# Optimization experiments

Measured on AMD Instinct MI355X. Metric: run time of the kernel, lower is better.

Reference implementation:

```python
import jax, jax.numpy as jnp
import numpy as np


def _bilinear_sample(tex, grid):
    """grid_sample, bilinear, align_corners=True, padding_mode='zeros'.
    tex: [C, Hin, Win]; grid: [B, Ho, Wo, 2] in [-1, 1] (x=width, y=height).
    Returns [B, C, Ho, Wo].
    """
    C, Hin, Win = tex.shape
    gx, gy = grid[..., 0], grid[..., 1]
    # align_corners=True mapping
    ix = (gx + 1.0) * 0.5 * (Win - 1)
    iy = (gy + 1.0) * 0.5 * (Hin - 1)
    ix0 = jnp.floor(ix)
    iy0 = jnp.floor(iy)
    wx1 = ix - ix0
    wy1 = iy - iy0
    wx0 = 1.0 - wx1
    wy0 = 1.0 - wy1

    def gather(iy_, ix_):
        valid = (ix_ >= 0) & (ix_ <= Win - 1) & (iy_ >= 0) & (iy_ <= Hin - 1)
        ic = jnp.clip(ix_, 0, Win - 1).astype(jnp.int32)
        jc = jnp.clip(iy_, 0, Hin - 1).astype(jnp.int32)
        v = tex[:, jc, ic]  # [C, B, Ho, Wo]
        return v * valid.astype(tex.dtype)[None]

    out = (gather(iy0, ix0) * (wy0 * wx0)[None]
           + gather(iy0, ix0 + 1) * (wy0 * wx1)[None]
           + gather(iy0 + 1, ix0) * (wy1 * wx0)[None]
           + gather(iy0 + 1, ix0 + 1) * (wy1 * wx1)[None])
    return jnp.transpose(out, (1, 0, 2, 3))  # [B, C, Ho, Wo]


def setup_inputs() -> dict:
    key = jax.random.key(0)
    k = jax.random.split(key, 6)
    B, C, W, H = 4, 16, 1024, 1024
    Ho, Wo = 512, 512
    return {
        "x": jax.random.uniform(k[0], (B, Ho, Wo, 2), dtype=jnp.float32),
        "x_msk": jax.random.uniform(k[1], (B, Ho, Wo), dtype=jnp.float32),
        "layer1": jax.random.normal(k[2], (C, W, H), dtype=jnp.float32),
        "layer2": jax.random.normal(k[3], (C, W // 2, H // 2), dtype=jnp.float32),
        "layer3": jax.random.normal(k[4], (C, W // 4, H // 4), dtype=jnp.float32),
        "layer4": jax.random.normal(k[5], (C, W // 8, H // 8), dtype=jnp.float32),
    }


def reference(x, x_msk, layer1, layer2, layer3, layer4):
    grid = x * 2.0 - 1.0
    y = (_bilinear_sample(layer1, grid)
         + _bilinear_sample(layer2, grid)
         + _bilinear_sample(layer3, grid)
         + _bilinear_sample(layer4, grid))
    return y * x_msk[:, None]
```

## Files before the change

### kernel.cpp

```cpp
#include <hip/hip_runtime.h>
#include <hip/hip_fp16.h>

#define CH 16
#define NPIX (4 * 512 * 512)
#define NBINS 4096
#define NBLK_SORT 256
#define PPB (NPIX / NBLK_SORT)
#define SEGS 16

__global__ __launch_bounds__(256) void interleave_all_kernel(
    const float* __restrict__ l1, const float* __restrict__ l2,
    const float* __restrict__ l3, const float* __restrict__ l4,
    __half* __restrict__ w1, __half* __restrict__ w2,
    __half* __restrict__ w3, __half* __restrict__ w4) {
  int g = blockIdx.x * blockDim.x + threadIdx.x;
  const float* src; __half* dst; int HW, p;
  if (g < 1048576)      { src = l1; dst = w1; HW = 1048576; p = g; }
  else if (g < 1310720) { src = l2; dst = w2; HW = 262144;  p = g - 1048576; }
  else if (g < 1376256) { src = l3; dst = w3; HW = 65536;   p = g - 1310720; }
  else                  { src = l4; dst = w4; HW = 16384;   p = g - 1376256; }
  union { __half h[CH]; uint4 u[2]; } pk;
#pragma unroll
  for (int c = 0; c < CH; ++c) pk.h[c] = __float2half(src[(size_t)c * HW + p]);
  uint4* d = (uint4*)(dst + (size_t)p * CH);
  d[0] = pk.u[0];
  d[1] = pk.u[1];
}

__device__ __forceinline__ void corner_fma(const __half* __restrict__ t,
                                           size_t texel, float w, float acc[CH]) {
  const uint4* q = (const uint4*)(t + texel * CH);
  union { uint4 u; __half2 h[4]; } a, b;
  a.u = q[0];
  b.u = q[1];
#pragma unroll
  for (int i = 0; i < 4; ++i) {
    float2 f = __half22float2(a.h[i]);
    acc[2 * i + 0] = fmaf(f.x, w, acc[2 * i + 0]);
    acc[2 * i + 1] = fmaf(f.y, w, acc[2 * i + 1]);
  }
#pragma unroll
  for (int i = 0; i < 4; ++i) {
    float2 f = __half22float2(b.h[i]);
    acc[8 + 2 * i + 0] = fmaf(f.x, w, acc[8 + 2 * i + 0]);
    acc[8 + 2 * i + 1] = fmaf(f.y, w, acc[8 + 2 * i + 1]);
  }
}

__device__ __forceinline__ void sample_hwc16(const __half* __restrict__ t, int W,
                                             float gx, float gy, float acc[CH]) {
  const float W1 = (float)(W - 1);
  float ix = (gx + 1.0f) * 0.5f * W1;
  float iy = (gy + 1.0f) * 0.5f * W1;
  float ix0f = floorf(ix), iy0f = floorf(iy);
  float wx1 = ix - ix0f, wy1 = iy - iy0f;
  float wx0 = 1.0f - wx1, wy0 = 1.0f - wy1;
  float ix1f = ix0f + 1.0f, iy1f = iy0f + 1.0f;
  float vx0 = (ix0f >= 0.0f && ix0f <= W1) ? 1.0f : 0.0f;
  float vx1 = (ix1f >= 0.0f && ix1f <= W1) ? 1.0f : 0.0f;
  float vy0 = (iy0f >= 0.0f && iy0f <= W1) ? 1.0f : 0.0f;
  float vy1 = (iy1f >= 0.0f && iy1f <= W1) ? 1.0f : 0.0f;
  int x0 = min(max((int)ix0f, 0), W - 1);
  int x1 = min(max((int)ix1f, 0), W - 1);
  int y0 = min(max((int)iy0f, 0), W - 1);
  int y1 = min(max((int)iy1f, 0), W - 1);
  float w00 = wy0 * wx0 * vy0 * vx0;
  float w01 = wy0 * wx1 * vy0 * vx1;
  float w10 = wy1 * wx0 * vy1 * vx0;
  float w11 = wy1 * wx1 * vy1 * vx1;
  corner_fma(t, (size_t)y0 * W + x0, w00, acc);
  corner_fma(t, (size_t)y0 * W + x1, w01, acc);
  corner_fma(t, (size_t)y1 * W + x0, w10, acc);
  corner_fma(t, (size_t)y1 * W + x1, w11, acc);
}

__device__ __forceinline__ int bin_of(float xv, float yv) {
  int bx = min(max((int)(xv * 1023.0f), 0), 1023) >> 4;
  int by = min(max((int)(yv * 1023.0f), 0), 1023) >> 4;
  return (by << 6) + bx;
}

__global__ __launch_bounds__(256) void hist_kernel(
    const float2* __restrict__ x, unsigned* __restrict__ hist) {
  __shared__ unsigned h[NBINS];
  int tid = threadIdx.x, blk = blockIdx.x;
#pragma unroll
  for (int i = 0; i < NBINS / 256; ++i) h[i * 256 + tid] = 0;
  __syncthreads();
  int base = blk * PPB;
#pragma unroll 4
  for (int c = 0; c < PPB / 256; ++c) {
    float2 g = x[base + c * 256 + tid];
    atomicAdd(&h[bin_of(g.x, g.y)], 1u);
  }
  __syncthreads();
#pragma unroll
  for (int i = 0; i < NBINS / 256; ++i)
    hist[(size_t)blk * NBINS + i * 256 + tid] = h[i * 256 + tid];
}

__global__ __launch_bounds__(256) void segsum_kernel(
    const unsigned* __restrict__ hist, unsigned* __restrict__ partial) {
  int gid = blockIdx.x * 256 + threadIdx.x;
  int s = gid >> 12, bin = gid & (NBINS - 1);
  unsigned sum = 0;
#pragma unroll
  for (int k = 0; k < NBLK_SORT / SEGS; ++k)
    sum += hist[(size_t)(s * (NBLK_SORT / SEGS) + k) * NBINS + bin];
  partial[gid] = sum;
}

__global__ __launch_bounds__(256) void segscan_kernel(
    unsigned* __restrict__ partial, unsigned* __restrict__ totals) {
  int bin = blockIdx.x * 256 + threadIdx.x;
  unsigned run = 0;
#pragma unroll
  for (int s = 0; s < SEGS; ++s) {
    unsigned v = partial[s * NBINS + bin];
    partial[s * NBINS + bin] = run;
    run += v;
  }
  totals[bin] = run;
}

__global__ __launch_bounds__(1024) void scan_kernel(
    const unsigned* __restrict__ counts, unsigned* __restrict__ cursor) {
  __shared__ unsigned part[1024];
  int t = threadIdx.x;
  unsigned c0 = counts[4 * t + 0], c1 = counts[4 * t + 1];
  unsigned c2 = counts[4 * t + 2], c3 = counts[4 * t + 3];
  part[t] = c0 + c1 + c2 + c3;
  __syncthreads();
  for (int off = 1; off < 1024; off <<= 1) {
    unsigned v = (t >= off) ? part[t - off] : 0u;
    __syncthreads();
    part[t] += v;
    __syncthreads();
  }
  unsigned base = (t > 0) ? part[t - 1] : 0u;
  cursor[4 * t + 0] = base;
  cursor[4 * t + 1] = base + c0;
  cursor[4 * t + 2] = base + c0 + c1;
  cursor[4 * t + 3] = base + c0 + c1 + c2;
}

__global__ __launch_bounds__(256) void colscan_kernel(
    unsigned* __restrict__ hist, const unsigned* __restrict__ partial,
    const unsigned* __restrict__ binbase) {
  int gid = blockIdx.x * 256 + threadIdx.x;
  int s = gid >> 12, bin = gid & (NBINS - 1);
  unsigned run = partial[s * NBINS + bin] + binbase[bin];
#pragma unroll
  for (int k = 0; k < NBLK_SORT / SEGS; ++k) {
    size_t idx = (size_t)(s * (NBLK_SORT / SEGS) + k) * NBINS + bin;
    unsigned v = hist[idx];
    hist[idx] = run;
    run += v;
  }
}

__global__ __launch_bounds__(256) void scatter2_kernel(
    const float2* __restrict__ x, const float* __restrict__ msk,
    const unsigned* __restrict__ hist, float4* __restrict__ pixrec) {
  __shared__ unsigned cur[NBINS];
  int tid = threadIdx.x, blk = blockIdx.x;
#pragma unroll
  for (int i = 0; i < NBINS / 256; ++i)
    cur[i * 256 + tid] = hist[(size_t)blk * NBINS + i * 256 + tid];
  __syncthreads();
  int base = blk * PPB;
#pragma unroll 4
  for (int c = 0; c < PPB / 256; ++c) {
    int p = base + c * 256 + tid;
    float2 g = x[p];
    float m = msk[p];
    unsigned i = atomicAdd(&cur[bin_of(g.x, g.y)], 1u);
    pixrec[i] = make_float4(g.x, g.y, __uint_as_float((unsigned)p), m);
  }
}

__device__ __forceinline__ unsigned spread4(unsigned v) {
  v = (v | (v << 2)) & 0x33u;
  v = (v | (v << 1)) & 0x55u;
  return v;
}

__global__ __launch_bounds__(256) void gather_binned_kernel(
    const float4* __restrict__ pixrec,
    const __half* __restrict__ t1, const __half* __restrict__ t2,
    const __half* __restrict__ t3, const __half* __restrict__ t4,
    __half* __restrict__ ws2) {
  __shared__ float4 srec[256];
  __shared__ unsigned scnt[256];
  __shared__ unsigned sbase[256];
  int tid = threadIdx.x;
  int bid = blockIdx.x;
  int swz = (bid & 7) * 512 + (bid >> 3);
  float4 r = pixrec[swz * 256 + tid];

  int txq = min(max((int)(r.x * 1023.0f), 0), 1023) & 15;
  int tyq = min(max((int)(r.y * 1023.0f), 0), 1023) & 15;
  unsigned key = spread4((unsigned)txq) | (spread4((unsigned)tyq) << 1);
  scnt[tid] = 0;
  __syncthreads();
  unsigned rank = atomicAdd(&scnt[key], 1u);
  __syncthreads();
  sbase[tid] = scnt[tid];
  __syncthreads();
  for (int off = 1; off < 256; off <<= 1) {
    unsigned v = (tid >= off) ? sbase[tid - off] : 0u;
    __syncthreads();
    sbase[tid] += v;
    __syncthreads();
  }
  unsigned pos = sbase[key] - scnt[key] + rank;
  srec[pos] = r;
  __syncthreads();
  r = srec[tid];

  float gx = r.x * 2.0f - 1.0f;
  float gy = r.y * 2.0f - 1.0f;
  unsigned p = __float_as_uint(r.z);
  float m = r.w;
  float acc[CH];
#pragma unroll
  for (int c = 0; c < CH; ++c) acc[c] = 0.0f;
  sample_hwc16(t1, 1024, gx, gy, acc);
  sample_hwc16(t2, 512, gx, gy, acc);
  sample_hwc16(t3, 256, gx, gy, acc);
  sample_hwc16(t4, 128, gx, gy, acc);
  union { __half2 h[8]; uint4 u[2]; } o;
#pragma unroll
  for (int c = 0; c < 8; ++c)
    o.h[c] = __floats2half2_rn(acc[2 * c] * m, acc[2 * c + 1] * m);
  uint4* w = (uint4*)(ws2 + (size_t)p * CH);
  w[0] = o.u[0];
  w[1] = o.u[1];
}

__global__ __launch_bounds__(256) void unscatter16_kernel(
    const __half* __restrict__ ws2, float* __restrict__ out) {
  int t = blockIdx.x * blockDim.x + threadIdx.x;
  int p0 = t * 4;
  int wo = p0 & 511, ho = (p0 >> 9) & 511, b = p0 >> 18;
  const uint4* s = (const uint4*)ws2;
  union { uint4 u[2]; __half2 h[8]; } v[4];
#pragma unroll
  for (int j = 0; j < 4; ++j) {
    v[j].u[0] = s[(size_t)(p0 + j) * 2 + 0];
    v[j].u[1] = s[(size_t)(p0 + j) * 2 + 1];
  }
  size_t obase = (size_t)b * (CH * 262144) + (size_t)ho * 512 + wo;
#pragma unroll
  for (int ch = 0; ch < CH; ++ch) {
    float4 o;
    o.x = __half2float(((ch & 1) ? __high2half(v[0].h[ch >> 1]) : __low2half(v[0].h[ch >> 1])));
    o.y = __half2float(((ch & 1) ? __high2half(v[1].h[ch >> 1]) : __low2half(v[1].h[ch >> 1])));
    o.z = __half2float(((ch & 1) ? __high2half(v[2].h[ch >> 1]) : __low2half(v[2].h[ch >> 1])));
    o.w = __half2float(((ch & 1) ? __high2half(v[3].h[ch >> 1]) : __low2half(v[3].h[ch >> 1])));
    *(float4*)(out + obase + (size_t)ch * 262144) = o;
  }
}

__global__ __launch_bounds__(256) void gather_hwc16_kernel(
    const float* __restrict__ x, const float* __restrict__ msk,
    const __half* __restrict__ t1, const __half* __restrict__ t2,
    const __half* __restrict__ t3, const __half* __restrict__ t4,
    float* __restrict__ out) {
  int p = blockIdx.x * blockDim.x + threadIdx.x;
  int wo = p & 511, ho = (p >> 9) & 511, b = p >> 18;
  float2 g = ((const float2*)x)[p];
  float gx = g.x * 2.0f - 1.0f;
  float gy = g.y * 2.0f - 1.0f;
  float m = msk[p];
  float acc[CH];
#pragma unroll
  for (int c = 0; c < CH; ++c) acc[c] = 0.0f;
  sample_hwc16(t1, 1024, gx, gy, acc);
  sample_hwc16(t2, 512, gx, gy, acc);
  sample_hwc16(t3, 256, gx, gy, acc);
  sample_hwc16(t4, 128, gx, gy, acc);
  size_t obase = (size_t)b * (CH * 262144) + (size_t)ho * 512 + wo;
#pragma unroll
  for (int c = 0; c < CH; ++c) out[obase + (size_t)c * 262144] = acc[c] * m;
}

__device__ __forceinline__ void sample_chw(const float* __restrict__ t, int W,
                                           float gx, float gy, float acc[CH]) {
  const float W1 = (float)(W - 1);
  float ix = (gx + 1.0f) * 0.5f * W1;
  float iy = (gy + 1.0f) * 0.5f * W1;
  float ix0f = floorf(ix), iy0f = floorf(iy);
  float wx1 = ix - ix0f, wy1 = iy - iy0f;
  float wx0 = 1.0f - wx1, wy0 = 1.0f - wy1;
  float ix1f = ix0f + 1.0f, iy1f = iy0f + 1.0f;
  float vx0 = (ix0f >= 0.0f && ix0f <= W1) ? 1.0f : 0.0f;
  float vx1 = (ix1f >= 0.0f && ix1f <= W1) ? 1.0f : 0.0f;
  float vy0 = (iy0f >= 0.0f && iy0f <= W1) ? 1.0f : 0.0f;
  float vy1 = (iy1f >= 0.0f && iy1f <= W1) ? 1.0f : 0.0f;
  int x0 = min(max((int)ix0f, 0), W - 1);
  int x1 = min(max((int)ix1f, 0), W - 1);
  int y0 = min(max((int)iy0f, 0), W - 1);
  int y1 = min(max((int)iy1f, 0), W - 1);
  float w00 = wy0 * wx0 * vy0 * vx0;
  float w01 = wy0 * wx1 * vy0 * vx1;
  float w10 = wy1 * wx0 * vy1 * vx0;
  float w11 = wy1 * wx1 * vy1 * vx1;
  size_t HW = (size_t)W * W;
  const float* b00 = t + (size_t)y0 * W + x0;
  const float* b01 = t + (size_t)y0 * W + x1;
  const float* b10 = t + (size_t)y1 * W + x0;
  const float* b11 = t + (size_t)y1 * W + x1;
#pragma unroll
  for (int c = 0; c < CH; ++c) {
    float v00 = b00[c * HW], v01 = b01[c * HW], v10 = b10[c * HW], v11 = b11[c * HW];
    acc[c] = fmaf(v00, w00, fmaf(v01, w01, fmaf(v10, w10, fmaf(v11, w11, acc[c]))));
  }
}

__global__ __launch_bounds__(256) void gather_chw_kernel(
    const float* __restrict__ x, const float* __restrict__ msk,
    const float* __restrict__ l1, const float* __restrict__ l2,
    const float* __restrict__ l3, const float* __restrict__ l4,
    float* __restrict__ out) {
  int p = blockIdx.x * blockDim.x + threadIdx.x;
  int wo = p & 511, ho = (p >> 9) & 511, b = p >> 18;
  float2 g = ((const float2*)x)[p];
  float gx = g.x * 2.0f - 1.0f;
  float gy = g.y * 2.0f - 1.0f;
  float m = msk[p];
  float acc[CH];
#pragma unroll
  for (int c = 0; c < CH; ++c) acc[c] = 0.0f;
  sample_chw(l1, 1024, gx, gy, acc);
  sample_chw(l2, 512, gx, gy, acc);
  sample_chw(l3, 256, gx, gy, acc);
  sample_chw(l4, 128, gx, gy, acc);
  size_t obase = (size_t)b * (CH * 262144) + (size_t)ho * 512 + wo;
#pragma unroll
  for (int c = 0; c < CH; ++c) out[obase + (size_t)c * 262144] = acc[c] * m;
}

extern "C" void kernel_launch(void* const* d_in, const int* in_sizes, int n_in,
                              void* d_out, int out_size, void* d_ws, size_t ws_size,
                              hipStream_t stream) {
  const float* x   = (const float*)d_in[0];
  const float* msk = (const float*)d_in[1];
  const float* l1  = (const float*)d_in[2];
  const float* l2  = (const float*)d_in[3];
  const float* l3  = (const float*)d_in[4];
  const float* l4  = (const float*)d_in[5];
  float* out = (float*)d_out;

  const size_t n_texel = 1048576 + 262144 + 65536 + 16384;
  const size_t tex_bytes = n_texel * CH * sizeof(__half);
  const size_t ws2_bytes = (size_t)NPIX * CH * sizeof(__half);
  const size_t rec_bytes = (size_t)NPIX * sizeof(float4);
  const size_t need_bin  = ws2_bytes + tex_bytes + rec_bytes;
  const size_t need_f16  = tex_bytes;

  if (ws_size >= need_bin) {
    char* base = (char*)d_ws;
    __half* ws2    = (__half*)base;
    __half* w1     = (__half*)(base + ws2_bytes);
    __half* w2     = w1 + (size_t)1048576 * CH;
    __half* w3     = w2 + (size_t)262144 * CH;
    __half* w4     = w3 + (size_t)65536 * CH;
    float4* pixrec = (float4*)(base + ws2_bytes + tex_bytes);
    unsigned* hist    = (unsigned*)base;
    unsigned* partial = hist + (size_t)NBLK_SORT * NBINS;
    unsigned* totals  = partial + (size_t)SEGS * NBINS;
    unsigned* binbase = totals + NBINS;

    interleave_all_kernel<<<(int)(n_texel / 256), 256, 0, stream>>>(
        l1, l2, l3, l4, w1, w2, w3, w4);
    hist_kernel<<<NBLK_SORT, 256, 0, stream>>>((const float2*)x, hist);
    segsum_kernel<<<SEGS * NBINS / 256, 256, 0, stream>>>(hist, partial);
    segscan_kernel<<<NBINS / 256, 256, 0, stream>>>(partial, totals);
    scan_kernel<<<1, 1024, 0, stream>>>(totals, binbase);
    colscan_kernel<<<SEGS * NBINS / 256, 256, 0, stream>>>(hist, partial, binbase);
    scatter2_kernel<<<NBLK_SORT, 256, 0, stream>>>((const float2*)x, msk, hist, pixrec);
    gather_binned_kernel<<<NPIX / 256, 256, 0, stream>>>(pixrec, w1, w2, w3, w4, ws2);
    unscatter16_kernel<<<NPIX / 4 / 256, 256, 0, stream>>>(ws2, out);
  } else if (ws_size >= need_f16) {
    __half* w1 = (__half*)d_ws;
    __half* w2 = w1 + (size_t)1048576 * CH;
    __half* w3 = w2 + (size_t)262144 * CH;
    __half* w4 = w3 + (size_t)65536 * CH;
    interleave_all_kernel<<<(int)(n_texel / 256), 256, 0, stream>>>(
        l1, l2, l3, l4, w1, w2, w3, w4);
    gather_hwc16_kernel<<<NPIX / 256, 256, 0, stream>>>(x, msk, w1, w2, w3, w4, out);
  } else {
    gather_chw_kernel<<<NPIX / 256, 256, 0, stream>>>(x, msk, l1, l2, l3, l4, out);
  }
}
```

Before: 124.8 us.

## Split binned gather across two threads per pixel, drop in-block Morton reorder

The binned gather kernel now assigns two threads per pixel, each handling 8 of the 16 half-precision channels with one 16-byte load per corner, and launches twice as many blocks. The in-block Morton-order sort (shared atomics, prefix scan, several barriers) is removed, leaving only the coarse bin ordering from the global sort. The aim is more memory-level parallelism, fewer registers per thread and less synchronisation overhead. The cost is that coordinate and weight math is repeated in both threads and the finer locality from the intra-block reorder is lost.

```diff
diff --git a/kernel.cpp b/kernel.cpp
--- a/kernel.cpp
+++ b/kernel.cpp
@@ -25,6 +25,47 @@
   uint4* d = (uint4*)(dst + (size_t)p * CH);
   d[0] = pk.u[0];
   d[1] = pk.u[1];
+}
+
+__device__ __forceinline__ void corner_fma_h(const __half* __restrict__ t,
+                                             size_t texel, int h, float w,
+                                             float acc[8]) {
+  union { uint4 u; __half2 hh[4]; } a;
+  a.u = ((const uint4*)t)[texel * 2 + h];
+#pragma unroll
+  for (int i = 0; i < 4; ++i) {
+    float2 f = __half22float2(a.hh[i]);
+    acc[2 * i + 0] = fmaf(f.x, w, acc[2 * i + 0]);
+    acc[2 * i + 1] = fmaf(f.y, w, acc[2 * i + 1]);
+  }
+}
+
+__device__ __forceinline__ void sample_hwc16h(const __half* __restrict__ t, int W,
+                                              float gx, float gy, int h,
+                                              float acc[8]) {
+  const float W1 = (float)(W - 1);
+  float ix = (gx + 1.0f) * 0.5f * W1;
+  float iy = (gy + 1.0f) * 0.5f * W1;
+  float ix0f = floorf(ix), iy0f = floorf(iy);
+  float wx1 = ix - ix0f, wy1 = iy - iy0f;
+  float wx0 = 1.0f - wx1, wy0 = 1.0f - wy1;
+  float ix1f = ix0f + 1.0f, iy1f = iy0f + 1.0f;
+  float vx0 = (ix0f >= 0.0f && ix0f <= W1) ? 1.0f : 0.0f;
+  float vx1 = (ix1f >= 0.0f && ix1f <= W1) ? 1.0f : 0.0f;
+  float vy0 = (iy0f >= 0.0f && iy0f <= W1) ? 1.0f : 0.0f;
+  float vy1 = (iy1f >= 0.0f && iy1f <= W1) ? 1.0f : 0.0f;
+  int x0 = min(max((int)ix0f, 0), W - 1);
+  int x1 = min(max((int)ix1f, 0), W - 1);
+  int y0 = min(max((int)iy0f, 0), W - 1);
+  int y1 = min(max((int)iy1f, 0), W - 1);
+  float w00 = wy0 * wx0 * vy0 * vx0;
+  float w01 = wy0 * wx1 * vy0 * vx1;
+  float w10 = wy1 * wx0 * vy1 * vx0;
+  float w11 = wy1 * wx1 * vy1 * vx1;
+  corner_fma_h(t, (size_t)y0 * W + x0, h, w00, acc);
+  corner_fma_h(t, (size_t)y0 * W + x1, h, w01, acc);
+  corner_fma_h(t, (size_t)y1 * W + x0, h, w10, acc);
+  corner_fma_h(t, (size_t)y1 * W + x1, h, w11, acc);
 }
 
 __device__ __forceinline__ void corner_fma(const __half* __restrict__ t,
@@ -179,63 +220,33 @@
   }
 }
 
-__device__ __forceinline__ unsigned spread4(unsigned v) {
-  v = (v | (v << 2)) & 0x33u;
-  v = (v | (v << 1)) & 0x55u;
-  return v;
-}
-
-__global__ __launch_bounds__(256) void gather_binned_kernel(
+__global__ __launch_bounds__(256) void gather_binned2_kernel(
     const float4* __restrict__ pixrec,
     const __half* __restrict__ t1, const __half* __restrict__ t2,
     const __half* __restrict__ t3, const __half* __restrict__ t4,
     __half* __restrict__ ws2) {
-  __shared__ float4 srec[256];
-  __shared__ unsigned scnt[256];
-  __shared__ unsigned sbase[256];
-  int tid = threadIdx.x;
   int bid = blockIdx.x;
-  int swz = (bid & 7) * 512 + (bid >> 3);
-  float4 r = pixrec[swz * 256 + tid];
-
-  int txq = min(max((int)(r.x * 1023.0f), 0), 1023) & 15;
-  int tyq = min(max((int)(r.y * 1023.0f), 0), 1023) & 15;
-  unsigned key = spread4((unsigned)txq) | (spread4((unsigned)tyq) << 1);
-  scnt[tid] = 0;
-  __syncthreads();
-  unsigned rank = atomicAdd(&scnt[key], 1u);
-  __syncthreads();
-  sbase[tid] = scnt[tid];
-  __syncthreads();
-  for (int off = 1; off < 256; off <<= 1) {
-    unsigned v = (tid >= off) ? sbase[tid - off] : 0u;
-    __syncthreads();
-    sbase[tid] += v;
-    __syncthreads();
-  }
-  unsigned pos = sbase[key] - scnt[key] + rank;
-  srec[pos] = r;
-  __syncthreads();
-  r = srec[tid];
-
+  int swz = (bid & 7) * 1024 + (bid >> 3);
+  int g = swz * 256 + threadIdx.x;
+  int i = g >> 1;
+  int h = g & 1;
+  float4 r = pixrec[i];
   float gx = r.x * 2.0f - 1.0f;
   float gy = r.y * 2.0f - 1.0f;
   unsigned p = __float_as_uint(r.z);
   float m = r.w;
-  float acc[CH];
-#pragma unroll
-  for (int c = 0; c < CH; ++c) acc[c] = 0.0f;
-  sample_hwc16(t1, 1024, gx, gy, acc);
-  sample_hwc16(t2, 512, gx, gy, acc);
-  sample_hwc16(t3, 256, gx, gy, acc);
-  sample_hwc16(t4, 128, gx, gy, acc);
-  union { __half2 h[8]; uint4 u[2]; } o;
-#pragma unroll
-  for (int c = 0; c < 8; ++c)
-    o.h[c] = __floats2half2_rn(acc[2 * c] * m, acc[2 * c + 1] * m);
-  uint4* w = (uint4*)(ws2 + (size_t)p * CH);
-  w[0] = o.u[0];
-  w[1] = o.u[1];
+  float acc[8];
+#pragma unroll
+  for (int c = 0; c < 8; ++c) acc[c] = 0.0f;
+  sample_hwc16h(t1, 1024, gx, gy, h, acc);
+  sample_hwc16h(t2, 512, gx, gy, h, acc);
+  sample_hwc16h(t3, 256, gx, gy, h, acc);
+  sample_hwc16h(t4, 128, gx, gy, h, acc);
+  union { __half2 hh[4]; uint4 u; } o;
+#pragma unroll
+  for (int c = 0; c < 4; ++c)
+    o.hh[c] = __floats2half2_rn(acc[2 * c] * m, acc[2 * c + 1] * m);
+  ((uint4*)(ws2 + (size_t)p * CH))[h] = o.u;
 }
 
 __global__ __launch_bounds__(256) void unscatter16_kernel(
@@ -380,7 +391,7 @@
     scan_kernel<<<1, 1024, 0, stream>>>(totals, binbase);
     colscan_kernel<<<SEGS * NBINS / 256, 256, 0, stream>>>(hist, partial, binbase);
     scatter2_kernel<<<NBLK_SORT, 256, 0, stream>>>((const float2*)x, msk, hist, pixrec);
-    gather_binned_kernel<<<NPIX / 256, 256, 0, stream>>>(pixrec, w1, w2, w3, w4, ws2);
+    gather_binned2_kernel<<<NPIX * 2 / 256, 256, 0, stream>>>(pixrec, w1, w2, w3, w4, ws2);
     unscatter16_kernel<<<NPIX / 4 / 256, 256, 0, stream>>>(ws2, out);
   } else if (ws_size >= need_f16) {
     __half* w1 = (__half*)d_ws;
```

After: 123.0 us. About the same (-1.5%).
